# Performance work log

Hardware: AMD Instinct MI355X
Metric: run time of the kernel (lower is better)

## Reference

```python
import jax, jax.numpy as jnp
import numpy as np
from jax import lax

B, L, IN, H, C = 32, 2048, 512, 512, 1000

def setup_inputs() -> dict:
    key = jax.random.key(0)
    ks = jax.random.split(key, 8)
    s_in = 1.0 / np.sqrt(IN)
    s_h = 1.0 / np.sqrt(H)
    return {
        "inputs": jax.random.normal(ks[0], (B, L, IN), jnp.float32),
        "hidden": jax.random.normal(ks[1], (B, L, H), jnp.float32),
        "Wi": jax.random.uniform(ks[2], (H, IN), jnp.float32, -s_in, s_in),
        "bi": jax.random.uniform(ks[3], (H,), jnp.float32, -s_in, s_in),
        "Wh": jax.random.uniform(ks[4], (H, H), jnp.float32, -s_h, s_h),
        "bh": jax.random.uniform(ks[5], (H,), jnp.float32, -s_h, s_h),
        "Wo": jax.random.uniform(ks[6], (C, H), jnp.float32, -s_h, s_h),
        "bo": jax.random.uniform(ks[7], (C,), jnp.float32, -s_h, s_h),
    }

def reference(inputs, hidden, Wi, bi, Wh, bh, Wo, bo):
    # Elman RNN: h_t = tanh(x_t Wi^T + bi + h_{t-1} Wh^T + bh)
    h0 = hidden[:, 0, :]                         # [B, H] initial state
    # Precompute input projection for all timesteps (same math, batched GEMM)
    x_proj = jnp.einsum('blh,oh->blo', inputs, Wi) + bi   # [B, L, H]
    xs = jnp.swapaxes(x_proj, 0, 1)              # [L, B, H]

    def step(h, xp_t):
        h_new = jnp.tanh(xp_t + h @ Wh.T + bh)
        return h_new, h_new

    _, hs = lax.scan(step, h0, xs)               # hs: [L, B, H]
    h_n = jnp.swapaxes(hs, 0, 1)                 # [B, L, H]
    output = jnp.einsum('blh,ch->blc', h_n, Wo) + bo  # [B, L, C]
    return output, h_n
```

## Files before the change

kernel.cpp:

```cpp
#include <hip/hip_runtime.h>

#define B_  32
#define L_  2048
#define IN_ 512
#define H_  512
#define C_  1000

typedef __bf16 bf16x8 __attribute__((ext_vector_type(8)));
typedef short  short8 __attribute__((ext_vector_type(8)));
typedef float  floatx4 __attribute__((ext_vector_type(4)));

__device__ __forceinline__ unsigned short f2bf(float x) {
    unsigned u = __builtin_bit_cast(unsigned, x);
    unsigned r = (u + 0x7fffu + ((u >> 16) & 1u)) >> 16;
    return (unsigned short)r;
}
__device__ __forceinline__ float bf2f(unsigned short s) {
    unsigned u = ((unsigned)s) << 16;
    return __builtin_bit_cast(float, u);
}

__global__ __launch_bounds__(256) void gemm_bias(
    const float* __restrict__ A, const float* __restrict__ W,
    const float* __restrict__ bias, float* __restrict__ Cc,
    int ldc, int Nreal)
{
    __shared__ unsigned short As[128 * 40];
    __shared__ unsigned short Bs[128 * 40];

    const int tid  = threadIdx.x;
    const int lane = tid & 63;
    const int wv   = tid >> 6;
    const int wm   = wv >> 1;
    const int wn   = wv & 1;
    const int quad = lane >> 4;
    const long mbase = (long)blockIdx.y * 128;
    const int  nbase = blockIdx.x * 128;

    floatx4 acc[4][4];
#pragma unroll
    for (int mt = 0; mt < 4; ++mt)
#pragma unroll
        for (int nt = 0; nt < 4; ++nt)
            acc[mt][nt] = (floatx4){0.f, 0.f, 0.f, 0.f};

    for (int kt = 0; kt < 16; ++kt) {
        const int kbase = kt * 32;
#pragma unroll
        for (int i = 0; i < 4; ++i) {
            const int f  = tid + i * 256;
            const int r  = f >> 3;
            const int c4 = f & 7;
            const float4 va = *(const float4*)(A + (mbase + r) * 512 + kbase + c4 * 4);
            unsigned alo = (unsigned)f2bf(va.x) | ((unsigned)f2bf(va.y) << 16);
            unsigned ahi = (unsigned)f2bf(va.z) | ((unsigned)f2bf(va.w) << 16);
            *(uint2*)(&As[r * 40 + c4 * 4]) = make_uint2(alo, ahi);

            const int n_g = nbase + r;
            float4 vb;
            if (n_g < Nreal) vb = *(const float4*)(W + (long)n_g * 512 + kbase + c4 * 4);
            else             vb = make_float4(0.f, 0.f, 0.f, 0.f);
            unsigned blo = (unsigned)f2bf(vb.x) | ((unsigned)f2bf(vb.y) << 16);
            unsigned bhi = (unsigned)f2bf(vb.z) | ((unsigned)f2bf(vb.w) << 16);
            *(uint2*)(&Bs[r * 40 + c4 * 4]) = make_uint2(blo, bhi);
        }
        __syncthreads();

        bf16x8 af[4], bfr[4];
#pragma unroll
        for (int mt = 0; mt < 4; ++mt)
            af[mt] = *(const bf16x8*)(&As[(wm * 64 + mt * 16 + (lane & 15)) * 40 + quad * 8]);
#pragma unroll
        for (int nt = 0; nt < 4; ++nt)
            bfr[nt] = *(const bf16x8*)(&Bs[(wn * 64 + nt * 16 + (lane & 15)) * 40 + quad * 8]);
#pragma unroll
        for (int mt = 0; mt < 4; ++mt)
#pragma unroll
            for (int nt = 0; nt < 4; ++nt)
                acc[mt][nt] = __builtin_amdgcn_mfma_f32_16x16x32_bf16(
                    af[mt], bfr[nt], acc[mt][nt], 0, 0, 0);
        __syncthreads();
    }

#pragma unroll
    for (int nt = 0; nt < 4; ++nt) {
        const int col = nbase + wn * 64 + nt * 16 + (lane & 15);
        if (col < Nreal) {
            const float bv = bias[col];
#pragma unroll
            for (int mt = 0; mt < 4; ++mt) {
#pragma unroll
                for (int i = 0; i < 4; ++i) {
                    const long row = mbase + wm * 64 + mt * 16 + quad * 4 + i;
                    Cc[row * (long)ldc + col] = acc[mt][nt][i] + bv;
                }
            }
        }
    }
}

__global__ __launch_bounds__(256, 1) void rnn_scan(
    const float* __restrict__ Wh, const float* __restrict__ bh,
    const float* __restrict__ hidden, const float* __restrict__ xp,
    float* __restrict__ hn, unsigned long long* exch)
{
    __shared__ unsigned short lds_hi[5 * 520];
    __shared__ unsigned short lds_lo[5 * 520];

    const int tid   = threadIdx.x;
    const int lane  = tid & 63;
    const int wv    = tid >> 6;
    const int wg    = blockIdx.x;
    const int group = wg >> 3;
    const int slice = wg & 7;
    const int b0    = group * 4;
    const int n0    = slice * 64;
    const int quad  = lane >> 4;
    const int rr    = ((lane & 15) < 4) ? (lane & 15) : 4;


    bf16x8 wf[16];
    {
        const int n_row = n0 + wv * 16 + (lane & 15);
#pragma unroll
        for (int kk = 0; kk < 16; ++kk) {
            const float4 w0 = *(const float4*)(Wh + (long)n_row * 512 + kk * 32 + quad * 8);
            const float4 w1 = *(const float4*)(Wh + (long)n_row * 512 + kk * 32 + quad * 8 + 4);
            short8 s;
            s[0] = (short)f2bf(w0.x); s[1] = (short)f2bf(w0.y);
            s[2] = (short)f2bf(w0.z); s[3] = (short)f2bf(w0.w);
            s[4] = (short)f2bf(w1.x); s[5] = (short)f2bf(w1.y);
            s[6] = (short)f2bf(w1.z); s[7] = (short)f2bf(w1.w);
            wf[kk] = __builtin_bit_cast(bf16x8, s);
        }
    }

    const int   n_lane = n0 + wv * 16 + (lane & 15);
    const int   b_lane = b0 + quad;
    const float bias_v = bh[n_lane];

    for (int i = tid; i < 520; i += 256) { lds_hi[4 * 520 + i] = 0; lds_lo[4 * 520 + i] = 0; }
#pragma unroll
    for (int i = 0; i < 8; ++i) {
        const int idx = tid + i * 256;
        const int r = idx >> 9, c = idx & 511;
        const float v = hidden[((long)(b0 + r) * L_) * H_ + c];
        const unsigned short hv = f2bf(v);
        lds_hi[r * 520 + c] = hv;
        lds_lo[r * 520 + c] = f2bf(v - bf2f(hv));
    }
    __syncthreads();

    for (int t = 0; t < L_; ++t) {
        const float xpv = xp[((long)b_lane * L_ + t) * H_ + n_lane];

        if (t > 0) {
            const unsigned tu = (unsigned)t;
            unsigned long long* src = exch + (size_t)(group * 2 + (t & 1)) * 2048;
            unsigned long long uv[8];
            unsigned pending = 0xffu;
            while (pending) {
#pragma unroll
                for (int i = 0; i < 8; ++i)
                    if (pending & (1u << i))
                        uv[i] = __hip_atomic_load(src + tid + i * 256,
                                                  __ATOMIC_RELAXED, __HIP_MEMORY_SCOPE_AGENT);
#pragma unroll
                for (int i = 0; i < 8; ++i)
                    if ((pending & (1u << i)) && (unsigned)(uv[i] >> 32) == tu)
                        pending &= ~(1u << i);
            }
#pragma unroll
            for (int i = 0; i < 8; ++i) {
                const int idx = tid + i * 256;
                const int r = idx >> 9, c = idx & 511;
                const float v = __builtin_bit_cast(float, (unsigned)(uv[i] & 0xffffffffu));
                const unsigned short hv = f2bf(v);
                lds_hi[r * 520 + c] = hv;
                lds_lo[r * 520 + c] = f2bf(v - bf2f(hv));
            }
        }
        __syncthreads();

        floatx4 a0 = (floatx4){0.f, 0.f, 0.f, 0.f};
        floatx4 a1 = (floatx4){0.f, 0.f, 0.f, 0.f};
#pragma unroll
        for (int kk = 0; kk < 16; ++kk) {
            const bf16x8 ah = *(const bf16x8*)(&lds_hi[rr * 520 + kk * 32 + quad * 8]);
            const bf16x8 al = *(const bf16x8*)(&lds_lo[rr * 520 + kk * 32 + quad * 8]);
            a0 = __builtin_amdgcn_mfma_f32_16x16x32_bf16(ah, wf[kk], a0, 0, 0, 0);
            a1 = __builtin_amdgcn_mfma_f32_16x16x32_bf16(al, wf[kk], a1, 0, 0, 0);
        }
        __syncthreads();

        const float c0 = a0[0] + a1[0], c1 = a0[1] + a1[1];
        const float c2 = a0[2] + a1[2], c3 = a0[3] + a1[3];
        const int srcl = lane & 15;
        const float s0 = __shfl(c0, srcl);
        const float s1 = __shfl(c1, srcl);
        const float s2 = __shfl(c2, srcl);
        const float s3 = __shfl(c3, srcl);
        float pre = (quad == 0) ? s0 : ((quad == 1) ? s1 : ((quad == 2) ? s2 : s3));
        pre += xpv + bias_v;
        const float e2 = __expf(pre + pre);
        const float hval = 1.0f - 2.0f / (e2 + 1.0f);

        {
            unsigned long long* dst = exch + (size_t)(group * 2 + ((t + 1) & 1)) * 2048
                                    + (size_t)quad * 512 + n_lane;
            const unsigned long long pk =
                ((unsigned long long)(unsigned)(t + 1) << 32) |
                (unsigned long long)__builtin_bit_cast(unsigned, hval);
            __hip_atomic_store(dst, pk, __ATOMIC_RELAXED, __HIP_MEMORY_SCOPE_AGENT);
        }

        hn[((long)b_lane * L_ + t) * H_ + n_lane] = hval;
    }
}

extern "C" void kernel_launch(void* const* d_in, const int* in_sizes, int n_in,
                              void* d_out, int out_size, void* d_ws, size_t ws_size,
                              hipStream_t stream)
{
    const float* inputs = (const float*)d_in[0];
    const float* hidden = (const float*)d_in[1];
    const float* Wi     = (const float*)d_in[2];
    const float* bi     = (const float*)d_in[3];
    const float* Wh     = (const float*)d_in[4];
    const float* bh     = (const float*)d_in[5];
    const float* Wo     = (const float*)d_in[6];
    const float* bo     = (const float*)d_in[7];

    float* out = (float*)d_out;
    float* xp  = out;
    float* hn  = out + (long)B_ * L_ * C_;

    hipMemsetAsync(d_ws, 0, (size_t)8 * 2 * 2048 * 8, stream);

    gemm_bias<<<dim3(4, 512), 256, 0, stream>>>(inputs, Wi, bi, xp, 512, 512);

    rnn_scan<<<dim3(64), 256, 0, stream>>>(Wh, bh, hidden, xp, hn,
                                           (unsigned long long*)d_ws);

    gemm_bias<<<dim3(8, 512), 256, 0, stream>>>(hn, Wo, bo, out, 1000, 1000);
}
```

Before: 5.686 ms.

## Stack hi/lo bf16 rows into one MFMA pass with double-buffered LDS

The hi and lo bf16 halves of the hidden state are stacked as extra M rows (rows 0-3 hi, rows 4-7 lo) of a single 16x16x32 MFMA. This halves the MFMA count per step, and the two partial sums are combined with a lane xor-shuffle. The hi/lo split moves to the producer, which packs both bf16 halves into the exchange word, so consumers only unpack shorts. The LDS buffer is double-buffered by step parity, which drops the second __syncthreads per timestep. The tradeoffs are more LDS use and an extra shuffle reduction on the serial critical path.

```diff
diff --git a/kernel.cpp b/kernel.cpp
--- a/kernel.cpp
+++ b/kernel.cpp
@@ -104,8 +104,7 @@
     const float* __restrict__ hidden, const float* __restrict__ xp,
     float* __restrict__ hn, unsigned long long* exch)
 {
-    __shared__ unsigned short lds_hi[5 * 520];
-    __shared__ unsigned short lds_lo[5 * 520];
+    __shared__ unsigned short lds_h[2][9 * 520];
 
     const int tid   = threadIdx.x;
     const int lane  = tid & 63;
@@ -116,7 +115,7 @@
     const int b0    = group * 4;
     const int n0    = slice * 64;
     const int quad  = lane >> 4;
-    const int rr    = ((lane & 15) < 4) ? (lane & 15) : 4;
+    const int rr    = ((lane & 15) < 8) ? (lane & 15) : 8;
 
 
     bf16x8 wf[16];
@@ -139,20 +138,24 @@
     const int   b_lane = b0 + quad;
     const float bias_v = bh[n_lane];
 
-    for (int i = tid; i < 520; i += 256) { lds_hi[4 * 520 + i] = 0; lds_lo[4 * 520 + i] = 0; }
+    for (int i = tid; i < 520; i += 256) {
+        lds_h[0][8 * 520 + i] = 0;
+        lds_h[1][8 * 520 + i] = 0;
+    }
 #pragma unroll
     for (int i = 0; i < 8; ++i) {
         const int idx = tid + i * 256;
         const int r = idx >> 9, c = idx & 511;
         const float v = hidden[((long)(b0 + r) * L_) * H_ + c];
         const unsigned short hv = f2bf(v);
-        lds_hi[r * 520 + c] = hv;
-        lds_lo[r * 520 + c] = f2bf(v - bf2f(hv));
-    }
-    __syncthreads();
+        lds_h[0][r * 520 + c]       = hv;
+        lds_h[0][(r + 4) * 520 + c] = f2bf(v - bf2f(hv));
+    }
 
     for (int t = 0; t < L_; ++t) {
         const float xpv = xp[((long)b_lane * L_ + t) * H_ + n_lane];
+
+        unsigned short* bufp = &lds_h[t & 1][0];
 
         if (t > 0) {
             const unsigned tu = (unsigned)t;
@@ -174,27 +177,32 @@
             for (int i = 0; i < 8; ++i) {
                 const int idx = tid + i * 256;
                 const int r = idx >> 9, c = idx & 511;
-                const float v = __builtin_bit_cast(float, (unsigned)(uv[i] & 0xffffffffu));
-                const unsigned short hv = f2bf(v);
-                lds_hi[r * 520 + c] = hv;
-                lds_lo[r * 520 + c] = f2bf(v - bf2f(hv));
+                const unsigned pv = (unsigned)(uv[i] & 0xffffffffu);
+                bufp[r * 520 + c]       = (unsigned short)(pv >> 16);
+                bufp[(r + 4) * 520 + c] = (unsigned short)(pv & 0xffffu);
             }
         }
         __syncthreads();
 
-        floatx4 a0 = (floatx4){0.f, 0.f, 0.f, 0.f};
-        floatx4 a1 = (floatx4){0.f, 0.f, 0.f, 0.f};
-#pragma unroll
-        for (int kk = 0; kk < 16; ++kk) {
-            const bf16x8 ah = *(const bf16x8*)(&lds_hi[rr * 520 + kk * 32 + quad * 8]);
-            const bf16x8 al = *(const bf16x8*)(&lds_lo[rr * 520 + kk * 32 + quad * 8]);
-            a0 = __builtin_amdgcn_mfma_f32_16x16x32_bf16(ah, wf[kk], a0, 0, 0, 0);
-            a1 = __builtin_amdgcn_mfma_f32_16x16x32_bf16(al, wf[kk], a1, 0, 0, 0);
-        }
-        __syncthreads();
-
-        const float c0 = a0[0] + a1[0], c1 = a0[1] + a1[1];
-        const float c2 = a0[2] + a1[2], c3 = a0[3] + a1[3];
+        bf16x8 fr[16];
+#pragma unroll
+        for (int kk = 0; kk < 16; ++kk)
+            fr[kk] = *(const bf16x8*)(&bufp[rr * 520 + kk * 32 + quad * 8]);
+
+        floatx4 ae = (floatx4){0.f, 0.f, 0.f, 0.f};
+        floatx4 ao = (floatx4){0.f, 0.f, 0.f, 0.f};
+#pragma unroll
+        for (int kk = 0; kk < 16; kk += 2) {
+            ae = __builtin_amdgcn_mfma_f32_16x16x32_bf16(fr[kk],     wf[kk],     ae, 0, 0, 0);
+            ao = __builtin_amdgcn_mfma_f32_16x16x32_bf16(fr[kk + 1], wf[kk + 1], ao, 0, 0, 0);
+        }
+
+        float c0 = ae[0] + ao[0], c1 = ae[1] + ao[1];
+        float c2 = ae[2] + ao[2], c3 = ae[3] + ao[3];
+        c0 += __shfl_xor(c0, 16);
+        c1 += __shfl_xor(c1, 16);
+        c2 += __shfl_xor(c2, 16);
+        c3 += __shfl_xor(c3, 16);
         const int srcl = lane & 15;
         const float s0 = __shfl(c0, srcl);
         const float s1 = __shfl(c1, srcl);
@@ -205,12 +213,16 @@
         const float e2 = __expf(pre + pre);
         const float hval = 1.0f - 2.0f / (e2 + 1.0f);
 
+        const unsigned short hv = f2bf(hval);
+        const unsigned short lv = f2bf(hval - bf2f(hv));
+
         {
             unsigned long long* dst = exch + (size_t)(group * 2 + ((t + 1) & 1)) * 2048
                                     + (size_t)quad * 512 + n_lane;
             const unsigned long long pk =
                 ((unsigned long long)(unsigned)(t + 1) << 32) |
-                (unsigned long long)__builtin_bit_cast(unsigned, hval);
+                ((unsigned long long)hv << 16) |
+                (unsigned long long)lv;
             __hip_atomic_store(dst, pk, __ATOMIC_RELAXED, __HIP_MEMORY_SCOPE_AGENT);
         }
 
```

Result: faster. 5.025 ms (-11.6%).
